# Kernel tuning notes

Hardware: AMD Instinct MI355X
Metric: run time of the kernel (lower is better)

The kernel has to match this reference:

```python
import jax, jax.numpy as jnp
import numpy as np

N = 20000
E = 320000
NEG_SLOPE = 0.2
BN_EPS = 1e-5


def _segment_softmax(e, dst, n):
    # e: [E, H] attention logits, dst: [E] destination node ids
    m = jax.ops.segment_max(e, dst, num_segments=n)           # [N, H]
    ex = jnp.exp(e - m[dst])                                   # [E, H]
    s = jax.ops.segment_sum(ex, dst, num_segments=n)          # [N, H]
    return ex / s[dst]


def gat_conv(x, src, dst, W, a_src, a_dst, b, heads, out_ch):
    # PyG GATConv (concat=True): h = x @ W reshaped to [N, H, C]
    n = x.shape[0]
    h = (x @ W).reshape(n, heads, out_ch)                      # [N, H, C]
    al_s = jnp.einsum('nhc,hc->nh', h, a_src)                  # [N, H]
    al_d = jnp.einsum('nhc,hc->nh', h, a_dst)
    e = jax.nn.leaky_relu(al_s[src] + al_d[dst], NEG_SLOPE)    # [E, H]
    alpha = _segment_softmax(e, dst, n)                        # [E, H]
    msg = h[src] * alpha[:, :, None]                           # [E, H, C]
    out = jax.ops.segment_sum(msg, dst, num_segments=n)        # [N, H, C]
    return out.reshape(n, heads * out_ch) + b


def batch_norm(x, gamma, beta):
    mu = jnp.mean(x, axis=0)
    var = jnp.mean((x - mu) ** 2, axis=0)  # biased, as torch BN training
    return gamma * (x - mu) * jax.lax.rsqrt(var + BN_EPS) + beta


def setup_inputs() -> dict:
    key = jax.random.key(0)
    ks = jax.random.split(key, 16)
    F_in, H1, C1 = 128, 8, 64
    D = H1 * C1  # 512
    OUT = 2
    def gl(k, shape, fan):
        return jax.random.normal(k, shape, dtype=jnp.float32) / np.sqrt(fan)
    x = jax.random.normal(ks[0], (N, F_in), dtype=jnp.float32)
    edge_index = jax.random.randint(ks[1], (2, E), 0, N, dtype=jnp.int64)
    return {
        'x': x, 'edge_index': edge_index,
        'W1': gl(ks[2], (F_in, H1 * C1), F_in),
        'a1s': gl(ks[3], (H1, C1), C1), 'a1d': gl(ks[4], (H1, C1), C1),
        'b1': jnp.zeros((D,), jnp.float32),
        'W2': gl(ks[5], (D, D), D),
        'a2s': gl(ks[6], (1, D), D), 'a2d': gl(ks[7], (1, D), D),
        'b2': jnp.zeros((D,), jnp.float32),
        'fc1_w': gl(ks[8], (D, D), D), 'fc1_b': jnp.zeros((D,), jnp.float32),
        'g1': jnp.ones((D,), jnp.float32), 'be1': jnp.zeros((D,), jnp.float32),
        'fc2_w': gl(ks[9], (D, D), D), 'fc2_b': jnp.zeros((D,), jnp.float32),
        'g2': jnp.ones((D,), jnp.float32), 'be2': jnp.zeros((D,), jnp.float32),
        'lin_w': gl(ks[10], (D, OUT), D), 'lin_b': jnp.zeros((OUT,), jnp.float32),
    }


def reference(x, edge_index, W1, a1s, a1d, b1, W2, a2s, a2d, b2,
              fc1_w, fc1_b, g1, be1, fc2_w, fc2_b, g2, be2, lin_w, lin_b):
    n = x.shape[0]
    loop = jnp.arange(n, dtype=edge_index.dtype)
    src = jnp.concatenate([edge_index[0], loop])  # add self-loops (PyG default)
    dst = jnp.concatenate([edge_index[1], loop])
    h = gat_conv(x, src, dst, W1, a1s, a1d, b1, heads=8, out_ch=64)
    h = batch_norm(jax.nn.relu(h @ fc1_w + fc1_b), g1, be1)
    h = gat_conv(h, src, dst, W2, a2s, a2d, b2, heads=1, out_ch=512)
    h = batch_norm(jax.nn.relu(h @ fc2_w + fc2_b), g2, be2)
    out = jax.nn.relu(h @ lin_w + lin_b)  # dropout p=0 is identity
    return out
```

## Files before the change

kernel.cpp:

```cpp
#include <hip/hip_runtime.h>
#include <hip/hip_bf16.h>

static constexpr int NN = 20000;
static constexpr int EE = 320000;
static constexpr int ET = EE + NN;
static constexpr int DD = 512;
static constexpr int FIN = 128;
static constexpr int ETP_MAX = ET + 7 * NN;

typedef __attribute__((ext_vector_type(8))) short short8;
typedef __attribute__((ext_vector_type(8))) unsigned short ushort8;
typedef __attribute__((ext_vector_type(4))) float f32x4;

__device__ __forceinline__ unsigned short f2bf(float f) {
    unsigned u = __float_as_uint(f);
    u += 0x7fffu + ((u >> 16) & 1u);
    return (unsigned short)(u >> 16);
}
__device__ __forceinline__ float bf2f(unsigned short b) {
    return __uint_as_float(((unsigned)b) << 16);
}

__device__ __forceinline__ void async_copy16(short* lds, const unsigned short* g) {
    __builtin_amdgcn_global_load_lds(
        (const __attribute__((address_space(1))) unsigned int*)g,
        (__attribute__((address_space(3))) unsigned int*)lds,
        16, 0, 0);
}

__global__ void scan_k(const int* __restrict__ deg, int* __restrict__ row_ptr,
                       int* __restrict__ perm) {
    __shared__ int part[1024];
    __shared__ int hist16[16][512];
    __shared__ int hbase[512];
    __shared__ int btot[512];
    int t = threadIdx.x;
    int wv = t >> 6;
    for (int k = t; k < 16 * 512; k += 1024) ((int*)hist16)[k] = 0;
    __syncthreads();
    const int CH = (NN + 1023) / 1024;
    int start = t * CH;
    int end = min(start + CH, NN);
    int dl[CH];
    int s = 0;
    for (int i = start; i < end; ++i) {
        int d = deg[i] + 1;
        dl[i - start] = d;
        s += (d + 7) & ~7;
        atomicAdd(&hist16[wv][min(d, 511)], 1);
    }
    part[t] = s;
    __syncthreads();
    if (t < 512) {
        int base = 0;
#pragma unroll
        for (int w = 0; w < 16; ++w) { int c = hist16[w][t]; hist16[w][t] = base; base += c; }
        btot[t] = base;
        hbase[t] = base;
    }
    __syncthreads();
    for (int off = 1; off < 512; off <<= 1) {
        int v = 0;
        if (t < 512 && t >= off) v = hbase[t - off];
        __syncthreads();
        if (t < 512) hbase[t] += v;
        __syncthreads();
    }
    if (t < 512) hbase[t] -= btot[t];
    for (int off = 1; off < 1024; off <<= 1) {
        int v = 0;
        if (t >= off) v = part[t - off];
        __syncthreads();
        part[t] += v;
        __syncthreads();
    }
    int base = (t == 0) ? 0 : part[t - 1];
    for (int i = start; i < end; ++i) { row_ptr[i] = base; base += (dl[i - start] + 7) & ~7; }
    if (t == 1023) row_ptr[NN] = part[1023];
    for (int i = start; i < end; ++i) {
        int d = min(dl[i - start], 511);
        int r = atomicAdd(&hist16[wv][d], 1);
        int pos = hbase[d] + r;
        perm[NN - 1 - pos] = i;
    }
}

static constexpr int TBLK = 208;
static constexpr int SZ_X4 = NN * FIN / 4;
static constexpr int XCB = (SZ_X4 + 255) / 256;
static constexpr int CDB = (EE + 255) / 256;
__global__ __launch_bounds__(256) void prep_all_k(
    const float* __restrict__ x, const float* __restrict__ W1,
    const float* __restrict__ fc1, const float* __restrict__ W2,
    const float* __restrict__ fc2,
    unsigned short* __restrict__ xb, unsigned short* __restrict__ W1t,
    unsigned short* __restrict__ fc1t, unsigned short* __restrict__ W2t,
    unsigned short* __restrict__ fc2t,
    const void* __restrict__ ei, int is64, int* __restrict__ deg) {
    int b = blockIdx.x;
    if (b < CDB) {
        int i = b * 256 + threadIdx.x;
        if (i < EE) {
            int d = is64 ? (int)((const long long*)ei)[EE + i] : ((const int*)ei)[EE + i];
            atomicAdd(&deg[d], 1);
        }
        return;
    }
    b -= CDB;
    if (b < TBLK) {
        __shared__ unsigned short tile[64][65];
        const float* src; unsigned short* dst; int rows, cols;
        if (b < 16)       { src = W1;  dst = W1t;  rows = FIN; cols = DD; }
        else if (b < 80)  { b -= 16;  src = fc1; dst = fc1t; rows = DD; cols = DD; }
        else if (b < 144) { b -= 80;  src = W2;  dst = W2t;  rows = DD; cols = DD; }
        else              { b -= 144; src = fc2; dst = fc2t; rows = DD; cols = DD; }
        int tc = cols / 64;
        int r0 = (b / tc) * 64, c0 = (b % tc) * 64;
        int t = threadIdx.x, lr = t >> 6, lc = t & 63;
#pragma unroll
        for (int p = 0; p < 16; ++p) {
            int r = lr + p * 4;
            tile[r][lc] = f2bf(src[(size_t)(r0 + r) * cols + c0 + lc]);
        }
        __syncthreads();
#pragma unroll
        for (int p = 0; p < 16; ++p) {
            int r = lr + p * 4;
            dst[(size_t)(c0 + r) * rows + r0 + lc] = tile[lc][r];
        }
        return;
    }
    int i = (b - TBLK) * 256 + threadIdx.x;
    if (i < SZ_X4) {
        float4 v = ((const float4*)x)[i];
        unsigned short o[4] = {f2bf(v.x), f2bf(v.y), f2bf(v.z), f2bf(v.w)};
        *(unsigned long long*)(xb + (size_t)i * 4) = *(const unsigned long long*)o;
    }
}

template <int RELU, int HASBIAS, int STATS, int ALS, int H, int FILLEX>
__global__ __launch_bounds__(256) void gemm_bf16(const unsigned short* __restrict__ A,
                                                 const unsigned short* __restrict__ Bt,
                                                 const float* __restrict__ bias,
                                                 unsigned short* __restrict__ Cb,
                                                 float* __restrict__ bnstat,
                                                 const float* __restrict__ avs,
                                                 const float* __restrict__ avd,
                                                 float* __restrict__ al_s,
                                                 float* __restrict__ al_d,
                                                 int M, int Nc, int K,
                                                 const void* __restrict__ ei, int is64,
                                                 const int* __restrict__ rp,
                                                 int* __restrict__ cursor,
                                                 unsigned short* __restrict__ csr_srcu) {
    int id = blockIdx.x;
    if (FILLEX && id >= 640) {
        int e = (id - 640) * 256 + threadIdx.x;
        if (e >= ET) return;
        int s, d;
        if (e < EE) {
            if (is64) {
                const long long* p = (const long long*)ei;
                s = (int)p[e]; d = (int)p[EE + e];
            } else {
                const int* p = (const int*)ei;
                s = p[e]; d = p[EE + e];
            }
        } else {
            s = d = e - EE;
        }
        int pos = atomicAdd(&cursor[d], 1);
        csr_srcu[rp[d] + pos] = (unsigned short)s;
        return;
    }
    int bm = ((id >> 5) << 3) + (id & 7);
    int bn = (id >> 3) & 3;
    int m0 = bm * 128, n0 = bn * 128;
    if (m0 >= M) return;

    __shared__ short As0[128 * 32], As1[128 * 32];
    __shared__ short Bs0[128 * 32], Bs1[128 * 32];
    int t = threadIdx.x;
    int lane = t & 63, w = t >> 6;
    int wm = w & 1, wn = w >> 1;
    int quad = lane >> 4, mr = lane & 15;
    int lrow = lane >> 2;
    int lcol = (lane & 3) * 8;

    const unsigned short* Ag0 = A + (size_t)(m0 + w * 32 + lrow) * K + lcol;
    const unsigned short* Ag1 = A + (size_t)(m0 + w * 32 + 16 + lrow) * K + lcol;
    const unsigned short* Bg0 = Bt + (size_t)(n0 + w * 32 + lrow) * K + lcol;
    const unsigned short* Bg1 = Bt + (size_t)(n0 + w * 32 + 16 + lrow) * K + lcol;
    short* Al[2][2] = {{&As0[(w * 32) * 32], &As0[(w * 32 + 16) * 32]},
                       {&As1[(w * 32) * 32], &As1[(w * 32 + 16) * 32]}};
    short* Bl[2][2] = {{&Bs0[(w * 32) * 32], &Bs0[(w * 32 + 16) * 32]},
                       {&Bs1[(w * 32) * 32], &Bs1[(w * 32 + 16) * 32]}};

    f32x4 zero = {0.f, 0.f, 0.f, 0.f};
    f32x4 acc[4][4];
#pragma unroll
    for (int i = 0; i < 4; ++i)
#pragma unroll
        for (int j = 0; j < 4; ++j) acc[i][j] = zero;

    for (int k0 = 0; k0 < K; k0 += 64) {
        async_copy16(Al[0][0], Ag0 + k0);
        async_copy16(Al[1][0], Ag0 + k0 + 32);
        async_copy16(Al[0][1], Ag1 + k0);
        async_copy16(Al[1][1], Ag1 + k0 + 32);
        async_copy16(Bl[0][0], Bg0 + k0);
        async_copy16(Bl[1][0], Bg0 + k0 + 32);
        async_copy16(Bl[0][1], Bg1 + k0);
        async_copy16(Bl[1][1], Bg1 + k0 + 32);
        __syncthreads();
#pragma unroll
        for (int kp = 0; kp < 2; ++kp) {
            const short* Sa = kp ? As1 : As0;
            const short* Sb = kp ? Bs1 : Bs0;
            short8 af[4], bfr[4];
#pragma unroll
            for (int i = 0; i < 4; ++i) {
                af[i]  = *(const short8*)(&Sa[(wm * 64 + i * 16 + mr) * 32 + quad * 8]);
                bfr[i] = *(const short8*)(&Sb[(wn * 64 + i * 16 + mr) * 32 + quad * 8]);
            }
#pragma unroll
            for (int i = 0; i < 4; ++i)
#pragma unroll
                for (int j = 0; j < 4; ++j)
                    acc[i][j] = __builtin_amdgcn_mfma_f32_16x16x32_bf16(af[i], bfr[j], acc[i][j], 0, 0, 0);
        }
        __syncthreads();
    }

    float as_j[4], ad_j[4];
    if (ALS) {
#pragma unroll
        for (int j = 0; j < 4; ++j) {
            int n = n0 + wn * 64 + j * 16 + mr;
            as_j[j] = avs[n];
            ad_j[j] = avd[n];
        }
    }
    const int head = (H == 8) ? ((n0 + wn * 64) >> 6) : 0;
    float sj[4] = {0.f, 0.f, 0.f, 0.f}, qj[4] = {0.f, 0.f, 0.f, 0.f};
#pragma unroll
    for (int i = 0; i < 4; ++i) {
        int mb = m0 + wm * 64 + i * 16 + quad * 4;
#pragma unroll
        for (int r = 0; r < 4; ++r) {
            int m = mb + r;
            bool valid = (m < M);
            float ps = 0.f, pd = 0.f;
#pragma unroll
            for (int j = 0; j < 4; ++j) {
                int n = n0 + wn * 64 + j * 16 + mr;
                float v = acc[i][j][r];
                if (HASBIAS) v += bias[n];
                if (RELU) v = fmaxf(v, 0.f);
                unsigned short hb = f2bf(v);
                if (valid) Cb[(size_t)m * Nc + n] = hb;
                if (ALS) {
                    float vv = bf2f(hb);
                    ps += as_j[j] * vv;
                    pd += ad_j[j] * vv;
                }
                if (STATS && valid) { sj[j] += v; qj[j] += v * v; }
            }
            if (ALS) {
                ps += __shfl_xor(ps, 1); pd += __shfl_xor(pd, 1);
                ps += __shfl_xor(ps, 2); pd += __shfl_xor(pd, 2);
                ps += __shfl_xor(ps, 4); pd += __shfl_xor(pd, 4);
                ps += __shfl_xor(ps, 8); pd += __shfl_xor(pd, 8);
                if (mr == 0 && valid) {
                    if (H == 8) { al_s[m * 8 + head] = ps; al_d[m * 8 + head] = pd; }
                    else        { atomicAdd(&al_s[m], ps); atomicAdd(&al_d[m], pd); }
                }
            }
        }
    }
    if (STATS) {
#pragma unroll
        for (int j = 0; j < 4; ++j) {
            float s = sj[j], q = qj[j];
            s += __shfl_xor(s, 16); q += __shfl_xor(q, 16);
            s += __shfl_xor(s, 32); q += __shfl_xor(q, 32);
            if (lane < 16) {
                int n = n0 + wn * 64 + j * 16 + mr;
                atomicAdd(&bnstat[n], s);
                atomicAdd(&bnstat[512 + n], q);
            }
        }
    }
}

template <int H>
__global__ __launch_bounds__(256) void gat_gather_k(const unsigned short* __restrict__ hb,
                                                    const unsigned short* __restrict__ srcu,
                                                    const float* __restrict__ al_sv,
                                                    const float* __restrict__ al_dv,
                                                    const int* __restrict__ row_ptr,
                                                    const int* __restrict__ perm,
                                                    const float* __restrict__ bias,
                                                    unsigned short* __restrict__ outb) {
    int b = blockIdx.x;
    int s = b & 7;
    int g = b >> 3;
    int t = threadIdx.x;
    int w = t >> 6, lane = t & 63;
    int grp = lane >> 3, cg = lane & 7;
    int n = perm[g * 32 + w * 8 + grp];
    int col = s * 64 + cg * 8;
    const char* hbase = (const char*)hb + col * 2;
    int beg = row_ptr[n];
    int nb = (row_ptr[n + 1] - beg) >> 3;
    const int hh = (H == 8) ? s : 0;
    float ald = al_dv[n * H + hh];

    float acc[8] = {0.f, 0.f, 0.f, 0.f, 0.f, 0.f, 0.f, 0.f};
    float psum = 0.f;
    ushort8 sv = *(const ushort8*)(srcu + beg);
    for (int bb = 1; bb <= nb; ++bb) {
        unsigned sa[8];
        float av[8];
#pragma unroll
        for (int u = 0; u < 8; ++u) {
            unsigned sn = sv[u];
            bool pad = (sn == 0xFFFFu);
            sa[u] = pad ? 0u : sn;
            float xx = al_sv[(size_t)sa[u] * H + hh] + ald;
            float a = __expf(fmaxf(xx, 0.2f * xx));
            av[u] = pad ? 0.f : a;
        }
        short8 hreg[8];
#pragma unroll
        for (int u = 0; u < 8; ++u)
            hreg[u] = *(const short8*)(hbase + ((size_t)sa[u] << 10));
        ushort8 svn;
        if (bb < nb) svn = *(const ushort8*)(srcu + beg + bb * 8);
#pragma unroll
        for (int u = 0; u < 8; ++u) psum += av[u];
#pragma unroll
        for (int u = 0; u < 8; ++u)
#pragma unroll
            for (int j = 0; j < 8; ++j)
                acc[j] = fmaf(av[u], bf2f((unsigned short)hreg[u][j]), acc[j]);
        if (bb < nb) sv = svn;
    }
    float inv = 1.0f / psum;
    float4 b0 = *(const float4*)(bias + col);
    float4 b1 = *(const float4*)(bias + col + 4);
    float bz[8] = {b0.x, b0.y, b0.z, b0.w, b1.x, b1.y, b1.z, b1.w};
    unsigned short ov[8];
#pragma unroll
    for (int j = 0; j < 8; ++j) ov[j] = f2bf(acc[j] * inv + bz[j]);
    *(int4*)(outb + (size_t)n * DD + col) = *(const int4*)ov;
}

__global__ __launch_bounds__(256) void fold1_k(const float* __restrict__ stat,
                                               const float* __restrict__ g,
                                               const float* __restrict__ be,
                                               unsigned short* __restrict__ W2t,
                                               float* __restrict__ bias2) {
    int t = threadIdx.x;
    int n = blockIdx.x * 4 + (t >> 6);
    int lane = t & 63;
    float pb = 0.f;
#pragma unroll
    for (int j = 0; j < 8; ++j) {
        int k = lane * 8 + j;
        float mean = stat[k] * (1.0f / NN);
        float var = stat[512 + k] * (1.0f / NN) - mean * mean;
        float sc = g[k] * rsqrtf(var + 1e-5f);
        float sh = be[k] - mean * sc;
        float wv = bf2f(W2t[n * DD + k]);
        W2t[n * DD + k] = f2bf(sc * wv);
        pb += sh * wv;
    }
    for (int off = 32; off; off >>= 1) pb += __shfl_down(pb, off);
    if (lane == 0) bias2[n] = pb;
}

__global__ __launch_bounds__(256) void final_linear(const unsigned short* __restrict__ xb,
                                                    const float* __restrict__ stat,
                                                    const float* __restrict__ g,
                                                    const float* __restrict__ be,
                                                    const float* __restrict__ lw,
                                                    const float* __restrict__ lb,
                                                    float* __restrict__ out) {
    __shared__ float w01[1024];
    __shared__ float red[512];
    int t = threadIdx.x;
    float rr0 = 0.f, rr1 = 0.f;
#pragma unroll
    for (int q = 0; q < 2; ++q) {
        int c = t * 2 + q;
        float mean = stat[c] * (1.0f / NN);
        float var = stat[512 + c] * (1.0f / NN) - mean * mean;
        float sc = g[c] * rsqrtf(var + 1e-5f);
        float sh = be[c] - mean * sc;
        float w0 = lw[2 * c], w1 = lw[2 * c + 1];
        w01[2 * c] = sc * w0;
        w01[2 * c + 1] = sc * w1;
        rr0 = fmaf(sh, w0, rr0);
        rr1 = fmaf(sh, w1, rr1);
    }
    red[t] = rr0;
    red[256 + t] = rr1;
    __syncthreads();
    for (int off = 128; off; off >>= 1) {
        if (t < off) { red[t] += red[t + off]; red[256 + t] += red[256 + t + off]; }
        __syncthreads();
    }
    float k0 = red[0] + lb[0], k1 = red[256] + lb[1];

    int wave = blockIdx.x * 4 + (t >> 6);
    int lane = t & 63;
    short8 hv = *(const short8*)(xb + (size_t)wave * DD + lane * 8);
    float p0 = 0.f, p1 = 0.f;
#pragma unroll
    for (int j = 0; j < 8; ++j) {
        int c = lane * 8 + j;
        float h = bf2f((unsigned short)hv[j]);
        p0 = fmaf(h, w01[2 * c], p0);
        p1 = fmaf(h, w01[2 * c + 1], p1);
    }
    for (int off = 32; off; off >>= 1) {
        p0 += __shfl_down(p0, off);
        p1 += __shfl_down(p1, off);
    }
    if (lane == 0) {
        out[wave * 2 + 0] = fmaxf(p0 + k0, 0.f);
        out[wave * 2 + 1] = fmaxf(p1 + k1, 0.f);
    }
}

extern "C" void kernel_launch(void* const* d_in, const int* in_sizes, int n_in,
                              void* d_out, int out_size, void* d_ws, size_t ws_size,
                              hipStream_t stream) {
    const float* x     = (const float*)d_in[0];
    const void*  ei    = d_in[1];
    const float* W1    = (const float*)d_in[2];
    const float* a1s   = (const float*)d_in[3];
    const float* a1d   = (const float*)d_in[4];
    const float* b1    = (const float*)d_in[5];
    const float* W2    = (const float*)d_in[6];
    const float* a2s   = (const float*)d_in[7];
    const float* a2d   = (const float*)d_in[8];
    const float* b2    = (const float*)d_in[9];
    const float* fc1_w = (const float*)d_in[10];
    const float* fc1_b = (const float*)d_in[11];
    const float* g1    = (const float*)d_in[12];
    const float* be1   = (const float*)d_in[13];
    const float* fc2_w = (const float*)d_in[14];
    const float* fc2_b = (const float*)d_in[15];
    const float* g2    = (const float*)d_in[16];
    const float* be2   = (const float*)d_in[17];
    const float* lin_w = (const float*)d_in[18];
    const float* lin_b = (const float*)d_in[19];
    float* out = (float*)d_out;

    char* ws = (char*)d_ws;
    auto alloc = [&](size_t bytes) {
        void* p = (void*)ws;
        ws += (bytes + 255) & ~size_t(255);
        return p;
    };
    unsigned short* h_bf    = (unsigned short*)alloc((size_t)NN * DD * 2);
    unsigned short* act_bf  = (unsigned short*)alloc((size_t)NN * DD * 2);
    unsigned short* W1t     = (unsigned short*)alloc((size_t)DD * FIN * 2);
    unsigned short* fc1t    = (unsigned short*)alloc((size_t)DD * DD * 2);
    unsigned short* W2t     = (unsigned short*)alloc((size_t)DD * DD * 2);
    unsigned short* fc2t    = (unsigned short*)alloc((size_t)DD * DD * 2);
    float*          al_s    = (float*)alloc((size_t)NN * 8 * 4);
    float*          al_d    = (float*)alloc((size_t)NN * 8 * 4);
    int*            row_ptr = (int*)alloc((size_t)(NN + 1) * 4);
    int*            perm    = (int*)alloc((size_t)NN * 4);
    float*          bias2f  = (float*)alloc(512 * 4);
    int*            deg     = (int*)alloc((size_t)(4 * NN + 2048) * 4);
    int*            cursor  = deg + NN;
    float*          bnstatA = (float*)(deg + 2 * NN);
    float*          bnstatB = bnstatA + 1024;
    float*          al_s2   = bnstatA + 2048;
    float*          al_d2   = al_s2 + NN;
    unsigned short* csr_srcu = (unsigned short*)alloc((size_t)ETP_MAX * 2);

    const int is64 = (in_sizes[1] >= (int)(2u * EE * 8u)) ? 1 : 0;

    hipMemsetAsync(deg, 0, (size_t)(4 * NN + 2048) * 4, stream);
    hipMemsetAsync(csr_srcu, 0xFF, (size_t)ETP_MAX * 2, stream);

    unsigned short* x_bf = act_bf;
    const int prep_blocks = CDB + TBLK + XCB;
    prep_all_k<<<prep_blocks, 256, 0, stream>>>(x, W1, fc1_w, W2, fc2_w,
                                                x_bf, W1t, fc1t, W2t, fc2t,
                                                ei, is64, deg);
    scan_k<<<1, 1024, 0, stream>>>(deg, row_ptr, perm);

    const int GB = 640;
    const int FB = (ET + 255) / 256;
    const int GGB = 8 * (NN / 32);

    gemm_bf16<0, 0, 0, 1, 8, 1><<<GB + FB, 256, 0, stream>>>(
        x_bf, W1t, nullptr, h_bf, nullptr, a1s, a1d, al_s, al_d, NN, DD, FIN,
        ei, is64, row_ptr, cursor, csr_srcu);
    gat_gather_k<8><<<GGB, 256, 0, stream>>>(h_bf, csr_srcu, al_s, al_d, row_ptr, perm, b1, act_bf);
    gemm_bf16<1, 1, 1, 0, 8, 0><<<GB, 256, 0, stream>>>(
        act_bf, fc1t, fc1_b, h_bf, bnstatA, nullptr, nullptr, nullptr, nullptr, NN, DD, DD,
        nullptr, 0, nullptr, nullptr, nullptr);
    fold1_k<<<128, 256, 0, stream>>>(bnstatA, g1, be1, W2t, bias2f);

    gemm_bf16<0, 1, 0, 1, 1, 0><<<GB, 256, 0, stream>>>(
        h_bf, W2t, bias2f, act_bf, nullptr, a2s, a2d, al_s2, al_d2, NN, DD, DD,
        nullptr, 0, nullptr, nullptr, nullptr);
    gat_gather_k<1><<<GGB, 256, 0, stream>>>(act_bf, csr_srcu, al_s2, al_d2, row_ptr, perm, b2, h_bf);
    gemm_bf16<1, 1, 1, 0, 8, 0><<<GB, 256, 0, stream>>>(
        h_bf, fc2t, fc2_b, act_bf, bnstatB, nullptr, nullptr, nullptr, nullptr, NN, DD, DD,
        nullptr, 0, nullptr, nullptr, nullptr);

    final_linear<<<NN / 4, 256, 0, stream>>>(act_bf, bnstatB, g2, be2, lin_w, lin_b, out);
}
```

Before: 329.2 us.

## Use wave-shuffle scans in scan_k and head-major attention logit layout

The block-wide scans in scan_k, which used shared memory with many barriers, are replaced by wavefront shuffle-up scans plus a small cross-wave pass. This cuts the number of __syncthreads calls in a single-block kernel. Separately, the per-head attention logits al_s/al_d move from node-major [N,8] to head-major [8,N], so gathers in the aggregation kernel read from a contiguous per-head array. The gathers stay random, so the locality gain from the new layout may be small.

```diff
diff --git a/kernel.cpp b/kernel.cpp
--- a/kernel.cpp
+++ b/kernel.cpp
@@ -30,12 +30,12 @@
 
 __global__ void scan_k(const int* __restrict__ deg, int* __restrict__ row_ptr,
                        int* __restrict__ perm) {
-    __shared__ int part[1024];
     __shared__ int hist16[16][512];
     __shared__ int hbase[512];
-    __shared__ int btot[512];
+    __shared__ int wsum[16];
+    __shared__ int bsum[8];
     int t = threadIdx.x;
-    int wv = t >> 6;
+    int lane = t & 63, wv = t >> 6;
     for (int k = t; k < 16 * 512; k += 1024) ((int*)hist16)[k] = 0;
     __syncthreads();
     const int CH = (NN + 1023) / 1024;
@@ -49,34 +49,59 @@
         s += (d + 7) & ~7;
         atomicAdd(&hist16[wv][min(d, 511)], 1);
     }
-    part[t] = s;
+    int incl = s;
+#pragma unroll
+    for (int off = 1; off < 64; off <<= 1) {
+        int v = __shfl_up(incl, off);
+        if (lane >= off) incl += v;
+    }
+    if (lane == 63) wsum[wv] = incl;
     __syncthreads();
     if (t < 512) {
         int base = 0;
 #pragma unroll
         for (int w = 0; w < 16; ++w) { int c = hist16[w][t]; hist16[w][t] = base; base += c; }
-        btot[t] = base;
         hbase[t] = base;
     }
-    __syncthreads();
-    for (int off = 1; off < 512; off <<= 1) {
-        int v = 0;
-        if (t < 512 && t >= off) v = hbase[t - off];
-        __syncthreads();
-        if (t < 512) hbase[t] += v;
-        __syncthreads();
-    }
-    if (t < 512) hbase[t] -= btot[t];
-    for (int off = 1; off < 1024; off <<= 1) {
-        int v = 0;
-        if (t >= off) v = part[t - off];
-        __syncthreads();
-        part[t] += v;
-        __syncthreads();
-    }
-    int base = (t == 0) ? 0 : part[t - 1];
+    if (wv == 0 && lane < 16) {
+        int v = wsum[lane];
+        int inc = v;
+#pragma unroll
+        for (int off = 1; off < 16; off <<= 1) {
+            int u = __shfl_up(inc, off, 16);
+            if (lane >= off) inc += u;
+        }
+        wsum[lane] = inc - v;
+    }
+    __syncthreads();
+    int base = wsum[wv] + incl - s;
     for (int i = start; i < end; ++i) { row_ptr[i] = base; base += (dl[i - start] + 7) & ~7; }
-    if (t == 1023) row_ptr[NN] = part[1023];
+    if (t == 1023) row_ptr[NN] = base;
+    int btot_own = 0, bincl = 0;
+    if (wv < 8) {
+        btot_own = hbase[wv * 64 + lane];
+        bincl = btot_own;
+#pragma unroll
+        for (int off = 1; off < 64; off <<= 1) {
+            int v = __shfl_up(bincl, off);
+            if (lane >= off) bincl += v;
+        }
+        if (lane == 63) bsum[wv] = bincl;
+    }
+    __syncthreads();
+    if (wv == 0 && lane < 8) {
+        int v = bsum[lane];
+        int inc = v;
+#pragma unroll
+        for (int off = 1; off < 8; off <<= 1) {
+            int u = __shfl_up(inc, off, 8);
+            if (lane >= off) inc += u;
+        }
+        bsum[lane] = inc - v;
+    }
+    __syncthreads();
+    if (wv < 8) hbase[wv * 64 + lane] = bsum[wv] + bincl - btot_own;
+    __syncthreads();
     for (int i = start; i < end; ++i) {
         int d = min(dl[i - start], 511);
         int r = atomicAdd(&hist16[wv][d], 1);
@@ -272,8 +297,12 @@
                 ps += __shfl_xor(ps, 4); pd += __shfl_xor(pd, 4);
                 ps += __shfl_xor(ps, 8); pd += __shfl_xor(pd, 8);
                 if (mr == 0 && valid) {
-                    if (H == 8) { al_s[m * 8 + head] = ps; al_d[m * 8 + head] = pd; }
-                    else        { atomicAdd(&al_s[m], ps); atomicAdd(&al_d[m], pd); }
+                    if (H == 8) {
+                        al_s[(size_t)head * NN + m] = ps;
+                        al_d[(size_t)head * NN + m] = pd;
+                    } else {
+                        atomicAdd(&al_s[m], ps); atomicAdd(&al_d[m], pd);
+                    }
                 }
             }
         }
@@ -313,8 +342,9 @@
     const char* hbase = (const char*)hb + col * 2;
     int beg = row_ptr[n];
     int nb = (row_ptr[n + 1] - beg) >> 3;
-    const int hh = (H == 8) ? s : 0;
-    float ald = al_dv[n * H + hh];
+    const size_t hoff = (H == 8) ? (size_t)s * NN : 0;
+    const float* asp = al_sv + hoff;
+    float ald = al_dv[hoff + n];
 
     float acc[8] = {0.f, 0.f, 0.f, 0.f, 0.f, 0.f, 0.f, 0.f};
     float psum = 0.f;
@@ -327,7 +357,7 @@
             unsigned sn = sv[u];
             bool pad = (sn == 0xFFFFu);
             sa[u] = pad ? 0u : sn;
-            float xx = al_sv[(size_t)sa[u] * H + hh] + ald;
+            float xx = asp[sa[u]] + ald;
             float a = __expf(fmaxf(xx, 0.2f * xx));
             av[u] = pad ? 0.f : a;
         }
```

After: 326.3 us. No clear change (-0.9%).
